# Kernel tuning notes

Measured on AMD Instinct MI355X. Metric: run time of the kernel, lower is better.

Reference implementation:

```python
import jax, jax.numpy as jnp
import numpy as np

N = 50000      # nodes
E = 800000     # edges (before self-loops)
DIN = 146      # input feature dim
D = 128        # hidden/out dim
G = 64         # graphs in batch
L = 4          # number of GCNConv layers (len(hidden_dims[1:]) + 1)
NC = 10        # classes
EPS = 1e-5     # BatchNorm eps


def setup_inputs() -> dict:
    key = jax.random.key(0)
    ks = jax.random.split(key, 12)
    x = jax.random.normal(ks[0], (N, DIN), jnp.float32)
    edge_index = jax.random.randint(ks[1], (2, E), 0, N, dtype=jnp.int64)
    batch = jnp.sort(jax.random.randint(ks[2], (N,), 0, G, dtype=jnp.int64))

    def lin(k, shape, fan_in):
        return (jax.random.normal(k, shape, jnp.float32) / np.sqrt(fan_in)).astype(jnp.float32)

    W_emb = lin(ks[3], (DIN, D), DIN)
    b_emb = jnp.zeros((D,), jnp.float32)
    W_gcn = lin(ks[4], (L, D, D), D)
    b_gcn = jnp.zeros((L, D), jnp.float32)
    bn_gamma = jnp.ones((L, D), jnp.float32)
    bn_beta = jnp.zeros((L, D), jnp.float32)
    W_r1 = lin(ks[5], (D, D // 2), D)
    b_r1 = jnp.zeros((D // 2,), jnp.float32)
    W_r2 = lin(ks[6], (D // 2, D // 4), D // 2)
    b_r2 = jnp.zeros((D // 4,), jnp.float32)
    W_r3 = lin(ks[7], (D // 4, NC), D // 4)
    b_r3 = jnp.zeros((NC,), jnp.float32)
    return {"x": x, "edge_index": edge_index, "batch": batch,
            "W_emb": W_emb, "b_emb": b_emb, "W_gcn": W_gcn, "b_gcn": b_gcn,
            "bn_gamma": bn_gamma, "bn_beta": bn_beta,
            "W_r1": W_r1, "b_r1": b_r1, "W_r2": W_r2, "b_r2": b_r2,
            "W_r3": W_r3, "b_r3": b_r3}


def reference(x, edge_index, batch, W_emb, b_emb, W_gcn, b_gcn,
              bn_gamma, bn_beta, W_r1, b_r1, W_r2, b_r2, W_r3, b_r3):
    # gcn_norm with self-loops (fill_value=1, improved=False)
    loop = jnp.arange(N, dtype=edge_index.dtype)
    src = jnp.concatenate([edge_index[0], loop])
    dst = jnp.concatenate([edge_index[1], loop])
    deg = jax.ops.segment_sum(jnp.ones(src.shape, x.dtype), dst, num_segments=N)
    dinv = jax.lax.rsqrt(jnp.maximum(deg, jnp.asarray(1e-12, x.dtype)))  # deg >= 1 (self loops)
    norm = (dinv[src] * dinv[dst])[:, None]  # [E+N, 1]

    h = x @ W_emb + b_emb  # embedding_h
    for l in range(L):
        h_in = h
        m = h @ W_gcn[l]                                            # [N, D]
        h = jax.ops.segment_sum(m[src] * norm, dst, num_segments=N) + b_gcn[l]
        # BatchNorm1d (training-mode batch stats, biased var)
        mu = h.mean(axis=0)
        var = h.var(axis=0)
        h = (h - mu) * jax.lax.rsqrt(var + EPS) * bn_gamma[l] + bn_beta[l]
        h = jax.nn.relu(h)
        h = h_in + h  # residual (dims always match here)

    # global_mean_pool over batch ids
    sums = jax.ops.segment_sum(h, batch, num_segments=G)
    cnts = jax.ops.segment_sum(jnp.ones((N, 1), h.dtype), batch, num_segments=G)
    hg = sums / jnp.maximum(cnts, 1.0)

    # MLPReadout: two hidden layers halving dims, then classifier
    z = jax.nn.relu(hg @ W_r1 + b_r1)
    z = jax.nn.relu(z @ W_r2 + b_r2)
    return z @ W_r3 + b_r3  # [G, NC]
```

## Files before the change

kernel.cpp:

```cpp
#include <hip/hip_runtime.h>
#include <hip/hip_bf16.h>

#define NN 50000
#define EE 800000
#define DIN 146
#define DD 128
#define GG 64
#define LL 4
#define NC 10
#define BN_EPS 1e-5f

#define KP_EMB 160
#define AST_L  136
#define NCOPY 64
#define NPW 4

#define NBKT 196
#define BHP  200
#define NBE  782

#define A_EDGE   NBE
#define A_INIT   (A_EDGE + 256)
#define A_REPACK (A_INIT + 3907)
#define A_BATCH  (A_REPACK + 196)
#define A_PARAMS (A_BATCH + 384)
#define A_WT     (A_PARAMS + 400)

#define B_GEMM 391
#define C_TOT  (B_GEMM + NBE)

typedef __attribute__((ext_vector_type(8))) short bf16x8;
typedef __attribute__((ext_vector_type(4))) float f32x4;

__device__ __forceinline__ float bf2f(__hip_bfloat16 v) { return __bfloat162float(v); }
__device__ __forceinline__ float loadf(const void* p, long i, int f32) {
    return f32 ? ((const float*)p)[i] : bf2f(((const __hip_bfloat16*)p)[i]);
}
__device__ __forceinline__ unsigned short f2bf_bits(float f) {
    __hip_bfloat16 h = __float2bfloat16(f);
    return *(unsigned short*)&h;
}
__device__ __forceinline__ float bfu2f(unsigned short u) {
    return __uint_as_float((unsigned)u << 16);
}
__device__ __forceinline__ float lo16(unsigned v) { return __uint_as_float(v << 16); }
__device__ __forceinline__ float hi16(unsigned v) { return __uint_as_float(v & 0xffff0000u); }
__device__ __forceinline__ ushort4 pack4(f32x4 v) {
    ushort4 u;
    u.x = f2bf_bits(v[0]); u.y = f2bf_bits(v[1]);
    u.z = f2bf_bits(v[2]); u.w = f2bf_bits(v[3]);
    return u;
}
__device__ __forceinline__ ushort4 pack4s(f32x4 v, float s) {
    ushort4 u;
    u.x = f2bf_bits(s * v[0]); u.y = f2bf_bits(s * v[1]);
    u.z = f2bf_bits(s * v[2]); u.w = f2bf_bits(s * v[3]);
    return u;
}

__device__ __forceinline__ int blk_excl_scan(int v, int t, int* wsum, int* total_sh) {
    __syncthreads();
    int lane = t & 63, w = t >> 6;
    int x = v;
    #pragma unroll
    for (int s = 1; s < 64; s <<= 1) {
        int y = __shfl_up(x, s, 64);
        if (lane >= s) x += y;
    }
    if (lane == 63) wsum[w] = x;
    __syncthreads();
    if (t == 0) {
        int a = 0;
        #pragma unroll
        for (int k = 0; k < 4; ++k) { int tmp = wsum[k]; wsum[k] = a; a += tmp; }
        *total_sh = a;
    }
    __syncthreads();
    return x - v + wsum[w];
}

__global__ void detect_kernel(const void* ei, const void* batch, const void* Wemb,
                              int* __restrict__ flags) {
    __shared__ int s_edge_nz, s_batch_nz, s_f32_cnt;
    int t = threadIdx.x;
    if (t == 0) { s_edge_nz = 0; s_batch_nz = 0; s_f32_cnt = 0; }
    __syncthreads();
    {   const int* w = (const int*)ei;
        long j = ((long)t * ((2L * EE) / 64)) | 1;
        if (w[j] != 0) atomicAdd(&s_edge_nz, 1);
    }
    {   const int* w = (const int*)batch;
        long j = ((long)(NN / 2) + (long)t * ((NN / 2) / 64)) | 1;
        if (j < NN && w[j] != 0) atomicAdd(&s_batch_nz, 1);
    }
    {   const unsigned short* w = (const unsigned short*)Wemb;
        unsigned short v = w[2 * t];
        int ex = (v >> 7) & 0xFF;
        if (v != 0 && ex >= 128) atomicAdd(&s_f32_cnt, 1);
    }
    __syncthreads();
    if (t == 0) {
        flags[0] = (s_edge_nz == 0) ? 1 : 0;
        flags[1] = (s_batch_nz == 0) ? 1 : 0;
        flags[2] = (s_f32_cnt >= 8) ? 1 : 0;
    }
}

struct Param { const void* src; float* dst; int src_n; int dst_n; };
struct Params12 { Param p[12]; };
struct WtDesc { const void* src; long src_off; unsigned short* dst; int K; int Kpad; };
struct WtDescs5 { WtDesc p[5]; };

__global__ __launch_bounds__(256) void mega_conv_kernel(
    const void* __restrict__ x, const void* __restrict__ ei,
    const void* __restrict__ batch, const int* __restrict__ flags,
    unsigned short* __restrict__ xb, float* __restrict__ statmulti,
    float* __restrict__ hgsum, int* __restrict__ b32,
    unsigned* __restrict__ pk, unsigned char* __restrict__ bkt,
    int* __restrict__ bh, int* __restrict__ dcnt, Params12 P, WtDescs5 W)
{
    int b = blockIdx.x;
    int t = threadIdx.x;
    if (b < A_EDGE) {
        __shared__ int hist[NBKT];
        if (t < NBKT) hist[t] = 0;
        __syncthreads();
        int e0 = (b * 256 + t) * 4;
        if (e0 < EE) {
            const int* w = (const int*)ei;
            int4 sv, dv;
            if (flags[0]) {
                int4 u0 = *(const int4*)(w + 2L * e0);
                int4 u1 = *(const int4*)(w + 2L * e0 + 4);
                int4 v0 = *(const int4*)(w + 2L * (EE + e0));
                int4 v1 = *(const int4*)(w + 2L * (EE + e0) + 4);
                sv = make_int4(u0.x, u0.z, u1.x, u1.z);
                dv = make_int4(v0.x, v0.z, v1.x, v1.z);
            } else {
                sv = *(const int4*)(w + e0);
                dv = *(const int4*)(w + EE + e0);
            }
            int ss[4] = {sv.x, sv.y, sv.z, sv.w};
            int dd2[4] = {dv.x, dv.y, dv.z, dv.w};
            unsigned pk4[4], bk4[4];
            #pragma unroll
            for (int k = 0; k < 4; ++k) {
                unsigned s = min((unsigned)ss[k], (unsigned)(NN - 1));
                unsigned d = min((unsigned)dd2[k], (unsigned)(NN - 1));
                pk4[k] = (s << 8) | (d & 255u);
                bk4[k] = d >> 8;
                atomicAdd(&hist[bk4[k]], 1);
            }
            *(uint4*)(pk + e0) = make_uint4(pk4[0], pk4[1], pk4[2], pk4[3]);
            *(uchar4*)(bkt + e0) = make_uchar4((unsigned char)bk4[0], (unsigned char)bk4[1],
                                               (unsigned char)bk4[2], (unsigned char)bk4[3]);
        }
        __syncthreads();
        if (t < NBKT) bh[b * BHP + t] = hist[t];
    } else if (b < A_INIT) {
        int i = (b - A_EDGE) * 256 + t;
        if (i == 0) *dcnt = 0;
        if (i < LL * NCOPY * 256) statmulti[i] = 0.0f;
        if (i < GG * DD) hgsum[i] = 0.0f;
    } else if (b < A_REPACK) {
        int f32 = flags[2];
        long idx8 = (long)(b - A_INIT) * 256 + t;
        if (idx8 < (long)NN * 20) {
            int row = (int)(idx8 / 20);
            int c8 = (int)(idx8 - (long)row * 20) * 8;
            float v[8];
            if (c8 + 8 <= DIN) {
                if (f32) {
                    const float* xp = (const float*)x + (long)row * DIN + c8;
                    #pragma unroll
                    for (int k2 = 0; k2 < 4; ++k2) {
                        float2 f = *(const float2*)(xp + 2 * k2);
                        v[2 * k2] = f.x; v[2 * k2 + 1] = f.y;
                    }
                } else {
                    const unsigned* xp = (const unsigned*)((const unsigned short*)x +
                                                           (long)row * DIN + c8);
                    #pragma unroll
                    for (int k2 = 0; k2 < 4; ++k2) {
                        unsigned u = xp[k2];
                        v[2 * k2] = bfu2f((unsigned short)u);
                        v[2 * k2 + 1] = bfu2f((unsigned short)(u >> 16));
                    }
                }
            } else {
                #pragma unroll
                for (int k = 0; k < 8; ++k) {
                    int col = c8 + k;
                    v[k] = (col < DIN) ? loadf(x, (long)row * DIN + col, f32) : 0.0f;
                }
            }
            unsigned o[4];
            #pragma unroll
            for (int k2 = 0; k2 < 4; ++k2)
                o[k2] = (unsigned)f2bf_bits(v[2 * k2]) |
                        ((unsigned)f2bf_bits(v[2 * k2 + 1]) << 16);
            *(uint4*)(xb + (long)row * KP_EMB + c8) = make_uint4(o[0], o[1], o[2], o[3]);
        }
    } else if (b < A_BATCH) {
        int i = (b - A_REPACK) * 256 + t;
        if (i < NN) b32[i] = flags[1] ? ((const int*)batch)[2L * i] : ((const int*)batch)[i];
    } else if (b < A_PARAMS) {
        int f32 = flags[2];
        int bb = b - A_BATCH;
        const Param& e = P.p[bb >> 5];
        int idx = (bb & 31) * 256 + t;
        if (idx < e.dst_n)
            e.dst[idx] = (idx < e.src_n) ? loadf(e.src, idx, f32) : 0.0f;
    } else {
        int f32 = flags[2];
        int bb = b - A_PARAMS;
        int y = bb / 80;
        const WtDesc& e = W.p[y];
        int idx = (bb - y * 80) * 256 + t;
        if (idx < 128 * e.Kpad) {
            int n = idx / e.Kpad, k = idx - n * e.Kpad;
            float v = (k < e.K) ? loadf(e.src, e.src_off + (long)k * DD + n, f32) : 0.0f;
            e.dst[idx] = f2bf_bits(v);
        }
    }
}

__global__ __launch_bounds__(256) void bscan_kernel(int* __restrict__ bh, int* __restrict__ tot,
                                                    int* __restrict__ base,
                                                    int* __restrict__ off_last,
                                                    int* __restrict__ dcnt) {
    __shared__ int wsum[4], total_sh;
    __shared__ int is_last;
    int b = blockIdx.x;
    int t = threadIdx.x;
    int carry = 0;
    #pragma unroll 1
    for (int c = 0; c < 4; ++c) {
        int i = c * 256 + t;
        int v = (i < NBE) ? bh[i * BHP + b] : 0;
        int excl = blk_excl_scan(v, t, wsum, &total_sh);
        if (i < NBE) bh[i * BHP + b] = excl + carry;
        carry += total_sh;
    }
    if (t == 0) {
        __hip_atomic_store(&tot[b], carry, __ATOMIC_RELEASE, __HIP_MEMORY_SCOPE_AGENT);
        int ticket = __hip_atomic_fetch_add(dcnt, 1, __ATOMIC_ACQ_REL, __HIP_MEMORY_SCOPE_AGENT);
        is_last = (ticket == NBKT - 1) ? 1 : 0;
    }
    __syncthreads();
    if (is_last) {
        int v = 0;
        if (t < NBKT)
            v = __hip_atomic_load(&tot[t], __ATOMIC_ACQUIRE, __HIP_MEMORY_SCOPE_AGENT);
        int excl = blk_excl_scan(v, t, wsum, &total_sh);
        if (t < NBKT) base[t] = excl;
        if (t == 0) { base[NBKT] = total_sh; *off_last = total_sh; }
    }
}


__global__ __launch_bounds__(256) void bucket_emb_kernel(
    const unsigned* __restrict__ pk, const unsigned char* __restrict__ bkt,
    const int* __restrict__ bh, const int* __restrict__ base,
    unsigned* __restrict__ bucketA,
    const unsigned short* __restrict__ Ab,
    const unsigned short* __restrict__ Wt,
    const float* __restrict__ bias,
    unsigned short* __restrict__ hb, int n)
{
    int t = threadIdx.x;
    if (blockIdx.x >= B_GEMM) {
        int bb = blockIdx.x - B_GEMM;
        __shared__ int cur[NBKT];
        if (t < NBKT) cur[t] = bh[bb * BHP + t] + base[t];
        __syncthreads();
        int e0 = (bb * 256 + t) * 4;
        if (e0 < EE) {
            uint4 p4 = *(const uint4*)(pk + e0);
            uchar4 b4 = *(const uchar4*)(bkt + e0);
            unsigned pks[4] = {p4.x, p4.y, p4.z, p4.w};
            unsigned bks[4] = {b4.x, b4.y, b4.z, b4.w};
            #pragma unroll
            for (int k = 0; k < 4; ++k) {
                int slot = atomicAdd(&cur[bks[k]], 1);
                bucketA[slot] = pks[k];
            }
        }
        return;
    }
    int r0 = blockIdx.x * 128;
    int lane = t & 63, w = t >> 6;
    int m = lane & 15, quad = lane >> 4;
    int rbase = r0 + w * 32;
    bf16x8 a[2][5];
    #pragma unroll
    for (int rt = 0; rt < 2; ++rt)
        #pragma unroll
        for (int c = 0; c < 5; ++c) {
            int rr = rbase + rt * 16 + m; if (rr > n - 1) rr = n - 1;
            a[rt][c] = *(const bf16x8*)(Ab + (long)rr * KP_EMB + c * 32 + quad * 8);
        }
    f32x4 acc[2][8];
    #pragma unroll
    for (int t8 = 0; t8 < 8; ++t8) {
        float4 bv = *(const float4*)&bias[t8 * 16 + quad * 4];
        f32x4 ai = {bv.x, bv.y, bv.z, bv.w};
        acc[0][t8] = ai; acc[1][t8] = ai;
    }
    #pragma unroll
    for (int t8 = 0; t8 < 8; ++t8) {
        #pragma unroll
        for (int c = 0; c < 5; ++c) {
            bf16x8 b = *(const bf16x8*)(Wt + (long)(t8 * 16 + m) * KP_EMB + c * 32 + quad * 8);
            acc[0][t8] = __builtin_amdgcn_mfma_f32_16x16x32_bf16(b, a[0][c], acc[0][t8], 0, 0, 0);
            acc[1][t8] = __builtin_amdgcn_mfma_f32_16x16x32_bf16(b, a[1][c], acc[1][t8], 0, 0, 0);
        }
    }
    #pragma unroll
    for (int rt = 0; rt < 2; ++rt) {
        int row = rbase + rt * 16 + m;
        if (row < n) {
            #pragma unroll
            for (int t8 = 0; t8 < 8; ++t8)
                *(ushort4*)(hb + (long)row * DD + t8 * 16 + quad * 4) = pack4(acc[rt][t8]);
        }
    }
}

__global__ __launch_bounds__(256) void csr_kernel(
    const unsigned* __restrict__ bucketA, const int* __restrict__ base,
    int* __restrict__ off, float* __restrict__ dinv, int* __restrict__ src_s)
{
    __shared__ int dg[256], cur[256], wsum[4], total_sh;
    int b = blockIdx.x, t = threadIdx.x;
    int eb0 = base[b], eb1 = base[b + 1];
    dg[t] = 0;
    __syncthreads();
    for (int e = eb0 + t; e < eb1; e += 256)
        atomicAdd(&dg[bucketA[e] & 255u], 1);
    __syncthreads();
    int v = dg[t];
    int excl = blk_excl_scan(v, t, wsum, &total_sh);
    int node = b * 256 + t;
    if (node < NN) {
        off[node] = eb0 + excl;
        dinv[node] = rsqrtf((float)(v + 1));
    }
    cur[t] = excl;
    __syncthreads();
    for (int e = eb0 + t; e < eb1; e += 256) {
        unsigned pv = bucketA[e];
        int r = atomicAdd(&cur[pv & 255u], 1);
        src_s[eb0 + r] = (int)(pv >> 8);
    }
}

__global__ __launch_bounds__(256) void gemm_plain_kernel(
    const unsigned short* __restrict__ Ab,
    const unsigned short* __restrict__ Wt,
    const float* __restrict__ dinv,
    unsigned short* __restrict__ Mb, int n)
{
    int t = threadIdx.x;
    int r0 = blockIdx.x * 128;
    int lane = t & 63, w = t >> 6;
    int m = lane & 15, quad = lane >> 4;
    int rbase = r0 + w * 32;
    bf16x8 a[2][4];
    #pragma unroll
    for (int rt = 0; rt < 2; ++rt)
        #pragma unroll
        for (int c = 0; c < 4; ++c) {
            int rr = rbase + rt * 16 + m; if (rr > n - 1) rr = n - 1;
            a[rt][c] = *(const bf16x8*)(Ab + (long)rr * DD + c * 32 + quad * 8);
        }
    float dvt[2];
    int rowt[2];
    #pragma unroll
    for (int rt = 0; rt < 2; ++rt) {
        int rr = rbase + rt * 16 + m;
        rowt[rt] = rr;
        if (rr > n - 1) rr = n - 1;
        dvt[rt] = dinv[rr];
    }
    f32x4 acc[2][8];
    #pragma unroll
    for (int t8 = 0; t8 < 8; ++t8) {
        f32x4 z = {0.f, 0.f, 0.f, 0.f};
        acc[0][t8] = z; acc[1][t8] = z;
    }
    #pragma unroll
    for (int t8 = 0; t8 < 8; ++t8) {
        #pragma unroll
        for (int c = 0; c < 4; ++c) {
            bf16x8 b = *(const bf16x8*)(Wt + (long)(t8 * 16 + m) * DD + c * 32 + quad * 8);
            acc[0][t8] = __builtin_amdgcn_mfma_f32_16x16x32_bf16(b, a[0][c], acc[0][t8], 0, 0, 0);
            acc[1][t8] = __builtin_amdgcn_mfma_f32_16x16x32_bf16(b, a[1][c], acc[1][t8], 0, 0, 0);
        }
    }
    #pragma unroll
    for (int rt = 0; rt < 2; ++rt) {
        if (rowt[rt] < n) {
            #pragma unroll
            for (int t8 = 0; t8 < 8; ++t8)
                *(ushort4*)(Mb + (long)rowt[rt] * DD + t8 * 16 + quad * 4) = pack4s(acc[rt][t8], dvt[rt]);
        }
    }
}

__global__ __launch_bounds__(256) void gemm_fused_kernel(
    const unsigned short* __restrict__ aggb, unsigned short* __restrict__ hb,
    const float* __restrict__ statmulti, const float* __restrict__ gamma,
    const float* __restrict__ beta, const float* __restrict__ dinv,
    const unsigned short* __restrict__ Wt, unsigned short* __restrict__ Mb, int n)
{
    __shared__ unsigned short As[128 * AST_L];
    __shared__ float bnsh[256];
    int t = threadIdx.x;
    int r0 = blockIdx.x * 128;
    {
        float s = 0.0f;
        #pragma unroll 8
        for (int k = 0; k < NCOPY; ++k) s += statmulti[k * 256 + t];
        bnsh[t] = s;
    }
    __syncthreads();
    {
        int c4 = (t & 31) * 4, rsub = t >> 5;
        float inv_n = 1.0f / (float)n;
        float4 sm = *(const float4*)&bnsh[c4];
        float4 sq = *(const float4*)&bnsh[128 + c4];
        float4 ga = *(const float4*)&gamma[c4];
        float4 be = *(const float4*)&beta[c4];
        float4 mu, rs;
        mu.x = sm.x * inv_n; mu.y = sm.y * inv_n; mu.z = sm.z * inv_n; mu.w = sm.w * inv_n;
        rs.x = rsqrtf(sq.x * inv_n - mu.x * mu.x + BN_EPS) * ga.x;
        rs.y = rsqrtf(sq.y * inv_n - mu.y * mu.y + BN_EPS) * ga.y;
        rs.z = rsqrtf(sq.z * inv_n - mu.z * mu.z + BN_EPS) * ga.z;
        rs.w = rsqrtf(sq.w * inv_n - mu.w * mu.w + BN_EPS) * ga.w;
        #pragma unroll 4
        for (int i = 0; i < 16; ++i) {
            int row = i * 8 + rsub;
            int r = r0 + row;
            unsigned short o0 = 0, o1 = 0, o2 = 0, o3 = 0;
            if (r < n) {
                long g = (long)r * DD + c4;
                ushort4 au = *(const ushort4*)&aggb[g];
                ushort4 hu = *(const ushort4*)&hb[g];
                float h0 = bfu2f(hu.x) + fmaxf((bfu2f(au.x) - mu.x) * rs.x + be.x, 0.0f);
                float h1 = bfu2f(hu.y) + fmaxf((bfu2f(au.y) - mu.y) * rs.y + be.y, 0.0f);
                float h2 = bfu2f(hu.z) + fmaxf((bfu2f(au.z) - mu.z) * rs.z + be.z, 0.0f);
                float h3 = bfu2f(hu.w) + fmaxf((bfu2f(au.w) - mu.w) * rs.w + be.w, 0.0f);
                o0 = f2bf_bits(h0); o1 = f2bf_bits(h1);
                o2 = f2bf_bits(h2); o3 = f2bf_bits(h3);
                ushort4 ho; ho.x = o0; ho.y = o1; ho.z = o2; ho.w = o3;
                *(ushort4*)&hb[g] = ho;
            }
            unsigned short* dst = &As[row * AST_L + c4];
            dst[0] = o0; dst[1] = o1; dst[2] = o2; dst[3] = o3;
        }
    }
    __syncthreads();
    int lane = t & 63, w = t >> 6;
    int m = lane & 15, quad = lane >> 4;
    int rl = w * 32;
    int rbase = r0 + rl;
    bf16x8 a[2][4];
    #pragma unroll
    for (int rt = 0; rt < 2; ++rt)
        #pragma unroll
        for (int c = 0; c < 4; ++c)
            a[rt][c] = *(const bf16x8*)(As + (rl + rt * 16 + m) * AST_L + c * 32 + quad * 8);
    float dvt[2];
    int rowt[2];
    #pragma unroll
    for (int rt = 0; rt < 2; ++rt) {
        int rr = rbase + rt * 16 + m;
        rowt[rt] = rr;
        if (rr > n - 1) rr = n - 1;
        dvt[rt] = dinv[rr];
    }
    f32x4 acc[2][8];
    #pragma unroll
    for (int t8 = 0; t8 < 8; ++t8) {
        f32x4 z = {0.f, 0.f, 0.f, 0.f};
        acc[0][t8] = z; acc[1][t8] = z;
    }
    #pragma unroll
    for (int t8 = 0; t8 < 8; ++t8) {
        #pragma unroll
        for (int c = 0; c < 4; ++c) {
            bf16x8 b = *(const bf16x8*)(Wt + (long)(t8 * 16 + m) * DD + c * 32 + quad * 8);
            acc[0][t8] = __builtin_amdgcn_mfma_f32_16x16x32_bf16(b, a[0][c], acc[0][t8], 0, 0, 0);
            acc[1][t8] = __builtin_amdgcn_mfma_f32_16x16x32_bf16(b, a[1][c], acc[1][t8], 0, 0, 0);
        }
    }
    #pragma unroll
    for (int rt = 0; rt < 2; ++rt) {
        if (rowt[rt] < n) {
            #pragma unroll
            for (int t8 = 0; t8 < 8; ++t8)
                *(ushort4*)(Mb + (long)rowt[rt] * DD + t8 * 16 + quad * 4) = pack4s(acc[rt][t8], dvt[rt]);
        }
    }
}

__global__ __launch_bounds__(256) void agg_kernel(
    const unsigned* __restrict__ mb32, const int* __restrict__ off,
    const int* __restrict__ src_s,
    const float* __restrict__ dinv, const float* __restrict__ bias,
    unsigned* __restrict__ aggb32, float* __restrict__ statacc)
{
    __shared__ float2 ssum[4][64], ssq[4][64];
    int t = threadIdx.x;
    int wv = t >> 6, lane = t & 63;
    float2 bi = ((const float2*)bias)[lane];
    float2 sAcc = {0.0f, 0.0f}, qAcc = {0.0f, 0.0f};
    int i0 = (blockIdx.x * 4 + wv) * NPW;
    #pragma unroll 1
    for (int ni = 0; ni < NPW; ++ni) {
        int i = i0 + ni;
        if (i >= NN) break;
        int e  = __builtin_amdgcn_readfirstlane(off[i]);
        int e1 = __builtin_amdgcn_readfirstlane(off[i + 1]);
        unsigned vs = mb32[(long)i * 64 + lane];
        float a0 = lo16(vs), a1 = hi16(vs);
        for (; e + 8 <= e1; e += 8) {
            int j0 = __builtin_amdgcn_readfirstlane(src_s[e + 0]);
            int j1 = __builtin_amdgcn_readfirstlane(src_s[e + 1]);
            int j2 = __builtin_amdgcn_readfirstlane(src_s[e + 2]);
            int j3 = __builtin_amdgcn_readfirstlane(src_s[e + 3]);
            int j4 = __builtin_amdgcn_readfirstlane(src_s[e + 4]);
            int j5 = __builtin_amdgcn_readfirstlane(src_s[e + 5]);
            int j6 = __builtin_amdgcn_readfirstlane(src_s[e + 6]);
            int j7 = __builtin_amdgcn_readfirstlane(src_s[e + 7]);
            unsigned v0 = mb32[(long)j0 * 64 + lane];
            unsigned v1 = mb32[(long)j1 * 64 + lane];
            unsigned v2 = mb32[(long)j2 * 64 + lane];
            unsigned v3 = mb32[(long)j3 * 64 + lane];
            unsigned v4 = mb32[(long)j4 * 64 + lane];
            unsigned v5 = mb32[(long)j5 * 64 + lane];
            unsigned v6 = mb32[(long)j6 * 64 + lane];
            unsigned v7 = mb32[(long)j7 * 64 + lane];
            a0 += lo16(v0); a1 += hi16(v0);
            a0 += lo16(v1); a1 += hi16(v1);
            a0 += lo16(v2); a1 += hi16(v2);
            a0 += lo16(v3); a1 += hi16(v3);
            a0 += lo16(v4); a1 += hi16(v4);
            a0 += lo16(v5); a1 += hi16(v5);
            a0 += lo16(v6); a1 += hi16(v6);
            a0 += lo16(v7); a1 += hi16(v7);
        }
        for (; e + 4 <= e1; e += 4) {
            int j0 = __builtin_amdgcn_readfirstlane(src_s[e + 0]);
            int j1 = __builtin_amdgcn_readfirstlane(src_s[e + 1]);
            int j2 = __builtin_amdgcn_readfirstlane(src_s[e + 2]);
            int j3 = __builtin_amdgcn_readfirstlane(src_s[e + 3]);
            unsigned v0 = mb32[(long)j0 * 64 + lane];
            unsigned v1 = mb32[(long)j1 * 64 + lane];
            unsigned v2 = mb32[(long)j2 * 64 + lane];
            unsigned v3 = mb32[(long)j3 * 64 + lane];
            a0 += lo16(v0); a1 += hi16(v0);
            a0 += lo16(v1); a1 += hi16(v1);
            a0 += lo16(v2); a1 += hi16(v2);
            a0 += lo16(v3); a1 += hi16(v3);
        }
        for (; e < e1; ++e) {
            int j = __builtin_amdgcn_readfirstlane(src_s[e]);
            unsigned v = mb32[(long)j * 64 + lane];
            a0 += lo16(v); a1 += hi16(v);
        }
        float di = dinv[i];
        float o0 = fmaf(di, a0, bi.x);
        float o1 = fmaf(di, a1, bi.y);
        aggb32[(long)i * 64 + lane] = ((unsigned)f2bf_bits(o1) << 16) | f2bf_bits(o0);
        sAcc.x += o0; sAcc.y += o1;
        qAcc.x += o0 * o0; qAcc.y += o1 * o1;
    }
    ssum[wv][lane] = sAcc; ssq[wv][lane] = qAcc;
    __syncthreads();
    if (wv == 0) {
        float2 s0 = ssum[0][lane], s1 = ssum[1][lane], s2 = ssum[2][lane], s3 = ssum[3][lane];
        float2 q0 = ssq[0][lane], q1 = ssq[1][lane], q2 = ssq[2][lane], q3 = ssq[3][lane];
        float sx = s0.x + s1.x + s2.x + s3.x;
        float sy = s0.y + s1.y + s2.y + s3.y;
        float qx = q0.x + q1.x + q2.x + q3.x;
        float qy = q0.y + q1.y + q2.y + q3.y;
        float* copy = statacc + (blockIdx.x & (NCOPY - 1)) * 256;
        atomicAdd(&copy[2 * lane], sx);
        atomicAdd(&copy[2 * lane + 1], sy);
        atomicAdd(&copy[128 + 2 * lane], qx);
        atomicAdd(&copy[128 + 2 * lane + 1], qy);
    }
}

__global__ void pool1_kernel(const unsigned short* __restrict__ hb,
                             const unsigned short* __restrict__ aggb,
                             const float* __restrict__ statmulti,
                             const float* __restrict__ gamma, const float* __restrict__ beta,
                             const int* __restrict__ b32, float* __restrict__ hgsum, int n) {
    __shared__ float bnsh[256];
    int t = threadIdx.x;
    {
        float s = 0.0f;
        #pragma unroll 8
        for (int k = 0; k < NCOPY; ++k) s += statmulti[k * 256 + t];
        bnsh[t] = s;
    }
    __syncthreads();
    int c4 = (t & 31) * 4, rsub = t >> 5;
    float inv_n = 1.0f / (float)n;
    float4 sm = *(const float4*)&bnsh[c4];
    float4 sq = *(const float4*)&bnsh[128 + c4];
    float4 ga = *(const float4*)&gamma[c4];
    float4 be = *(const float4*)&beta[c4];
    float4 mu, rs;
    mu.x = sm.x * inv_n; mu.y = sm.y * inv_n; mu.z = sm.z * inv_n; mu.w = sm.w * inv_n;
    rs.x = rsqrtf(sq.x * inv_n - mu.x * mu.x + BN_EPS) * ga.x;
    rs.y = rsqrtf(sq.y * inv_n - mu.y * mu.y + BN_EPS) * ga.y;
    rs.z = rsqrtf(sq.z * inv_n - mu.z * mu.z + BN_EPS) * ga.z;
    rs.w = rsqrtf(sq.w * inv_n - mu.w * mu.w + BN_EPS) * ga.w;
    int rows_pb = (n + gridDim.x - 1) / gridDim.x;
    int r0 = blockIdx.x * rows_pb;
    int r1 = min(n, r0 + rows_pb);
    float4 acc = {0, 0, 0, 0};
    int gcur = -1;
    for (int r = r0 + rsub; r < r1; r += 8) {
        int g = b32[r];
        if (g != gcur) {
            if (gcur >= 0) {
                atomicAdd(&hgsum[gcur * DD + c4 + 0], acc.x);
                atomicAdd(&hgsum[gcur * DD + c4 + 1], acc.y);
                atomicAdd(&hgsum[gcur * DD + c4 + 2], acc.z);
                atomicAdd(&hgsum[gcur * DD + c4 + 3], acc.w);
            }
            acc.x = acc.y = acc.z = acc.w = 0.0f;
            gcur = ((unsigned)g < (unsigned)GG) ? g : -1;
        }
        if (gcur >= 0) {
            long ix = (long)r * DD + c4;
            ushort4 au = *(const ushort4*)&aggb[ix];
            ushort4 hu = *(const ushort4*)&hb[ix];
            acc.x += bfu2f(hu.x) + fmaxf((bfu2f(au.x) - mu.x) * rs.x + be.x, 0.0f);
            acc.y += bfu2f(hu.y) + fmaxf((bfu2f(au.y) - mu.y) * rs.y + be.y, 0.0f);
            acc.z += bfu2f(hu.z) + fmaxf((bfu2f(au.z) - mu.z) * rs.z + be.z, 0.0f);
            acc.w += bfu2f(hu.w) + fmaxf((bfu2f(au.w) - mu.w) * rs.w + be.w, 0.0f);
        }
    }
    if (gcur >= 0) {
        atomicAdd(&hgsum[gcur * DD + c4 + 0], acc.x);
        atomicAdd(&hgsum[gcur * DD + c4 + 1], acc.y);
        atomicAdd(&hgsum[gcur * DD + c4 + 2], acc.z);
        atomicAdd(&hgsum[gcur * DD + c4 + 3], acc.w);
    }
}

__device__ int lower_bound_i(const int* __restrict__ a, int n, int v) {
    int lo = 0, hi = n;
    while (lo < hi) {
        int mid = (lo + hi) >> 1;
        if (a[mid] < v) lo = mid + 1; else hi = mid;
    }
    return lo;
}

__global__ void readout_kernel(const float* __restrict__ hgsum, const int* __restrict__ b32,
                               const float* __restrict__ W1, const float* __restrict__ b1,
                               const float* __restrict__ W2, const float* __restrict__ b2,
                               const float* __restrict__ W3, const float* __restrict__ b3,
                               const int* __restrict__ flags, void* __restrict__ out, int n) {
    int f32 = flags[2];
    int g = blockIdx.x;
    int t = threadIdx.x;
    __shared__ float hgs[DD];
    __shared__ float z1[DD / 2];
    __shared__ float z2[DD / 4];
    int lo = lower_bound_i(b32, n, g);
    int hi = lower_bound_i(b32, n, g + 1);
    float invc = 1.0f / fmaxf((float)(hi - lo), 1.0f);
    hgs[t] = hgsum[g * DD + t] * invc;
    __syncthreads();
    if (t < DD / 2) {
        float acc = b1[t];
        #pragma unroll 8
        for (int k = 0; k < DD; ++k) acc = fmaf(hgs[k], W1[k * (DD / 2) + t], acc);
        z1[t] = fmaxf(acc, 0.0f);
    }
    __syncthreads();
    if (t < DD / 4) {
        float acc = b2[t];
        #pragma unroll 8
        for (int k = 0; k < DD / 2; ++k) acc = fmaf(z1[k], W2[k * (DD / 4) + t], acc);
        z2[t] = fmaxf(acc, 0.0f);
    }
    __syncthreads();
    if (t < NC) {
        float acc = b3[t];
        #pragma unroll 8
        for (int k = 0; k < DD / 4; ++k) acc = fmaf(z2[k], W3[k * NC + t], acc);
        if (f32) ((float*)out)[g * NC + t] = acc;
        else     ((__hip_bfloat16*)out)[g * NC + t] = __float2bfloat16(acc);
    }
}

extern "C" void kernel_launch(void* const* d_in, const int* in_sizes, int n_in,
                              void* d_out, int out_size, void* d_ws, size_t ws_size,
                              hipStream_t stream) {
    const void* x      = d_in[0];
    const void* ei     = d_in[1];
    const void* batch  = d_in[2];
    const void* W_emb  = d_in[3];
    const void* b_emb  = d_in[4];
    const void* W_gcn  = d_in[5];
    const void* b_gcn  = d_in[6];
    const void* bn_g   = d_in[7];
    const void* bn_b   = d_in[8];
    const void* W_r1   = d_in[9];
    const void* b_r1   = d_in[10];
    const void* W_r2   = d_in[11];
    const void* b_r2   = d_in[12];
    const void* W_r3   = d_in[13];
    const void* b_r3   = d_in[14];

    char* p = (char*)d_ws;
    auto alloc = [&](size_t bytes) -> void* {
        void* r = (void*)p;
        p += (bytes + 255) & ~(size_t)255;
        return r;
    };
    int*   flags  = (int*)alloc(64 * 4);
    int*   dcnt   = (int*)alloc(64 * 4);
    float* statmulti = (float*)alloc((size_t)LL * NCOPY * 256 * 4);
    float* hgsum  = (float*)alloc((size_t)GG * DD * 4);
    int*   off    = (int*)alloc((size_t)(NN + 1) * 4);
    float* dinv   = (float*)alloc((size_t)NN * 4);
    int*   b32    = (int*)alloc((size_t)NN * 4);
    int*   src_s  = (int*)alloc((size_t)EE * 4);
    unsigned* pk  = (unsigned*)alloc((size_t)EE * 4);
    unsigned char* bkt = (unsigned char*)alloc((size_t)EE);
    int*   bh     = (int*)alloc((size_t)NBE * BHP * 4);
    int*   tot    = (int*)alloc(256 * 4);
    int*   base   = (int*)alloc(256 * 4);
    unsigned* bucketA = (unsigned*)alloc((size_t)EE * 4);
    unsigned short* hb = (unsigned short*)alloc((size_t)NN * DD * 2);
    unsigned short* mb = (unsigned short*)alloc((size_t)NN * DD * 2);
    unsigned short* aggb = (unsigned short*)alloc((size_t)NN * DD * 2);
    unsigned short* xb = (unsigned short*)alloc((size_t)NN * KP_EMB * 2);
    unsigned short* wt_emb = (unsigned short*)alloc((size_t)DD * KP_EMB * 2);
    unsigned short* wt_gcn = (unsigned short*)alloc((size_t)LL * DD * DD * 2);
    float* b_emb32 = (float*)alloc(DD * 4);
    float* b_gcn32 = (float*)alloc((size_t)LL * DD * 4);
    float* bng32   = (float*)alloc((size_t)LL * DD * 4);
    float* bnb32   = (float*)alloc((size_t)LL * DD * 4);
    float* wr1     = (float*)alloc((size_t)DD * (DD / 2) * 4);
    float* br1     = (float*)alloc((DD / 2) * 4);
    float* wr2     = (float*)alloc((size_t)(DD / 2) * (DD / 4) * 4);
    float* br2     = (float*)alloc((DD / 4) * 4);
    float* wr3     = (float*)alloc((size_t)(DD / 4) * NC * 4);
    float* br3     = (float*)alloc(NC * 4);

    detect_kernel<<<1, 64, 0, stream>>>(ei, batch, W_emb, flags);

    Params12 P;
    P.p[0]  = { b_emb, b_emb32, DD, DD };
    P.p[1]  = { b_gcn, b_gcn32, LL * DD, LL * DD };
    P.p[2]  = { bn_g,  bng32,   LL * DD, LL * DD };
    P.p[3]  = { bn_b,  bnb32,   LL * DD, LL * DD };
    P.p[4]  = { W_r1,  wr1,     DD * (DD / 2), DD * (DD / 2) };
    P.p[5]  = { b_r1,  br1,     DD / 2, DD / 2 };
    P.p[6]  = { W_r2,  wr2,     (DD / 2) * (DD / 4), (DD / 2) * (DD / 4) };
    P.p[7]  = { b_r2,  br2,     DD / 4, DD / 4 };
    P.p[8]  = { W_r3,  wr3,     (DD / 4) * NC, (DD / 4) * NC };
    P.p[9]  = { b_r3,  br3,     NC, NC };
    P.p[10] = { b_r3,  br3,     0, 0 };
    P.p[11] = { b_r3,  br3,     0, 0 };

    WtDescs5 W;
    W.p[0] = { W_emb, 0,            wt_emb,                DIN, KP_EMB };
    W.p[1] = { W_gcn, 0L * DD * DD, wt_gcn + 0L * DD * DD, DD,  DD };
    W.p[2] = { W_gcn, 1L * DD * DD, wt_gcn + 1L * DD * DD, DD,  DD };
    W.p[3] = { W_gcn, 2L * DD * DD, wt_gcn + 2L * DD * DD, DD,  DD };
    W.p[4] = { W_gcn, 3L * DD * DD, wt_gcn + 3L * DD * DD, DD,  DD };

    mega_conv_kernel<<<A_WT, 256, 0, stream>>>(x, ei, batch, flags, xb, statmulti,
                                               hgsum, b32, pk, bkt, bh, dcnt, P, W);

    bscan_kernel<<<NBKT, 256, 0, stream>>>(bh, tot, base, off + NN, dcnt);

    bucket_emb_kernel<<<C_TOT, 256, 0, stream>>>(pk, bkt, bh, base, bucketA,
                                                 xb, wt_emb, b_emb32, hb, NN);

    csr_kernel<<<NBKT, 256, 0, stream>>>(bucketA, base, off, dinv, src_s);

    gemm_plain_kernel<<<(NN + 127) / 128, 256, 0, stream>>>(hb, wt_gcn, dinv, mb, NN);

    int ngemm = (NN + 127) / 128;
    int nagg = (NN + 4 * NPW - 1) / (4 * NPW);
    for (int l = 0; l < LL; ++l) {
        if (l > 0) {
            gemm_fused_kernel<<<ngemm, 256, 0, stream>>>(
                aggb, hb, statmulti + (size_t)(l - 1) * NCOPY * 256,
                bng32 + (l - 1) * DD, bnb32 + (l - 1) * DD,
                dinv, wt_gcn + (size_t)l * DD * DD, mb, NN);
        }
        agg_kernel<<<nagg, 256, 0, stream>>>((const unsigned*)mb, off, src_s, dinv,
                                             b_gcn32 + l * DD, (unsigned*)aggb,
                                             statmulti + (size_t)l * NCOPY * 256);
    }

    pool1_kernel<<<512, 256, 0, stream>>>(hb, aggb, statmulti + (size_t)(LL - 1) * NCOPY * 256,
                                          bng32 + (LL - 1) * DD, bnb32 + (LL - 1) * DD,
                                          b32, hgsum, NN);
    readout_kernel<<<GG, DD, 0, stream>>>(hgsum, b32, wr1, br1, wr2, br2, wr3, br3,
                                          flags, d_out, NN);
}
```

Before: 402.0 us.

## Fuse first GCN GEMM into embedding kernel; apply source dinv inside aggregation

The first layer's GEMM moves into the embedding kernel. The embedding output is staged in shared memory and multiplied by W_gcn[0] in the same block, so the separate gemm_plain launch and its reread of h go away. Because dinv is not ready until csr_kernel runs after this point, the GEMMs no longer pre-scale rows by dinv. Instead the aggregation kernel loads dinv[src] per edge through scalar loads and uses FMAs, which adds a scalar load per edge. Nodes per wave in the aggregation are halved to give it more blocks.

```diff
diff --git a/kernel.cpp b/kernel.cpp
--- a/kernel.cpp
+++ b/kernel.cpp
@@ -13,7 +13,7 @@
 #define KP_EMB 160
 #define AST_L  136
 #define NCOPY 64
-#define NPW 4
+#define NPW 2
 
 #define NBKT 196
 #define BHP  200
@@ -45,16 +45,13 @@
 }
 __device__ __forceinline__ float lo16(unsigned v) { return __uint_as_float(v << 16); }
 __device__ __forceinline__ float hi16(unsigned v) { return __uint_as_float(v & 0xffff0000u); }
+__device__ __forceinline__ float sload_f(const float* __restrict__ p, int j) {
+    return __uint_as_float(__builtin_amdgcn_readfirstlane(__float_as_uint(p[j])));
+}
 __device__ __forceinline__ ushort4 pack4(f32x4 v) {
     ushort4 u;
     u.x = f2bf_bits(v[0]); u.y = f2bf_bits(v[1]);
     u.z = f2bf_bits(v[2]); u.w = f2bf_bits(v[3]);
-    return u;
-}
-__device__ __forceinline__ ushort4 pack4s(f32x4 v, float s) {
-    ushort4 u;
-    u.x = f2bf_bits(s * v[0]); u.y = f2bf_bits(s * v[1]);
-    u.z = f2bf_bits(s * v[2]); u.w = f2bf_bits(s * v[3]);
     return u;
 }
 
@@ -265,14 +262,19 @@
     unsigned* __restrict__ bucketA,
     const unsigned short* __restrict__ Ab,
     const unsigned short* __restrict__ Wt,
+    const unsigned short* __restrict__ Wt0,
     const float* __restrict__ bias,
-    unsigned short* __restrict__ hb, int n)
+    unsigned short* __restrict__ hb,
+    unsigned short* __restrict__ Mb, int n)
 {
+    __shared__ union {
+        unsigned short As[128 * AST_L];
+        int cur[NBKT];
+    } sh;
     int t = threadIdx.x;
     if (blockIdx.x >= B_GEMM) {
         int bb = blockIdx.x - B_GEMM;
-        __shared__ int cur[NBKT];
-        if (t < NBKT) cur[t] = bh[bb * BHP + t] + base[t];
+        if (t < NBKT) sh.cur[t] = bh[bb * BHP + t] + base[t];
         __syncthreads();
         int e0 = (bb * 256 + t) * 4;
         if (e0 < EE) {
@@ -282,7 +284,7 @@
             unsigned bks[4] = {b4.x, b4.y, b4.z, b4.w};
             #pragma unroll
             for (int k = 0; k < 4; ++k) {
-                int slot = atomicAdd(&cur[bks[k]], 1);
+                int slot = atomicAdd(&sh.cur[bks[k]], 1);
                 bucketA[slot] = pks[k];
             }
         }
@@ -291,7 +293,8 @@
     int r0 = blockIdx.x * 128;
     int lane = t & 63, w = t >> 6;
     int m = lane & 15, quad = lane >> 4;
-    int rbase = r0 + w * 32;
+    int rl = w * 32;
+    int rbase = r0 + rl;
     bf16x8 a[2][5];
     #pragma unroll
     for (int rt = 0; rt < 2; ++rt)
@@ -319,10 +322,44 @@
     #pragma unroll
     for (int rt = 0; rt < 2; ++rt) {
         int row = rbase + rt * 16 + m;
+        int rloc = rl + rt * 16 + m;
+        #pragma unroll
+        for (int t8 = 0; t8 < 8; ++t8) {
+            ushort4 u = pack4(acc[rt][t8]);
+            *(ushort4*)(&sh.As[rloc * AST_L + t8 * 16 + quad * 4]) = u;
+            if (row < n)
+                *(ushort4*)(hb + (long)row * DD + t8 * 16 + quad * 4) = u;
+        }
+    }
+    __syncthreads();
+    bf16x8 a2[2][4];
+    #pragma unroll
+    for (int rt = 0; rt < 2; ++rt)
+        #pragma unroll
+        for (int c = 0; c < 4; ++c)
+            a2[rt][c] = *(const bf16x8*)(&sh.As[(rl + rt * 16 + m) * AST_L + c * 32 + quad * 8]);
+    f32x4 acc2[2][8];
+    #pragma unroll
+    for (int t8 = 0; t8 < 8; ++t8) {
+        f32x4 z = {0.f, 0.f, 0.f, 0.f};
+        acc2[0][t8] = z; acc2[1][t8] = z;
+    }
+    #pragma unroll
+    for (int t8 = 0; t8 < 8; ++t8) {
+        #pragma unroll
+        for (int c = 0; c < 4; ++c) {
+            bf16x8 b = *(const bf16x8*)(Wt0 + (long)(t8 * 16 + m) * DD + c * 32 + quad * 8);
+            acc2[0][t8] = __builtin_amdgcn_mfma_f32_16x16x32_bf16(b, a2[0][c], acc2[0][t8], 0, 0, 0);
+            acc2[1][t8] = __builtin_amdgcn_mfma_f32_16x16x32_bf16(b, a2[1][c], acc2[1][t8], 0, 0, 0);
+        }
+    }
+    #pragma unroll
+    for (int rt = 0; rt < 2; ++rt) {
+        int row = rbase + rt * 16 + m;
         if (row < n) {
             #pragma unroll
             for (int t8 = 0; t8 < 8; ++t8)
-                *(ushort4*)(hb + (long)row * DD + t8 * 16 + quad * 4) = pack4(acc[rt][t8]);
+                *(ushort4*)(Mb + (long)row * DD + t8 * 16 + quad * 4) = pack4(acc2[rt][t8]);
         }
     }
 }
@@ -355,63 +392,10 @@
     }
 }
 
-__global__ __launch_bounds__(256) void gemm_plain_kernel(
-    const unsigned short* __restrict__ Ab,
-    const unsigned short* __restrict__ Wt,
-    const float* __restrict__ dinv,
-    unsigned short* __restrict__ Mb, int n)
-{
-    int t = threadIdx.x;
-    int r0 = blockIdx.x * 128;
-    int lane = t & 63, w = t >> 6;
-    int m = lane & 15, quad = lane >> 4;
-    int rbase = r0 + w * 32;
-    bf16x8 a[2][4];
-    #pragma unroll
-    for (int rt = 0; rt < 2; ++rt)
-        #pragma unroll
-        for (int c = 0; c < 4; ++c) {
-            int rr = rbase + rt * 16 + m; if (rr > n - 1) rr = n - 1;
-            a[rt][c] = *(const bf16x8*)(Ab + (long)rr * DD + c * 32 + quad * 8);
-        }
-    float dvt[2];
-    int rowt[2];
-    #pragma unroll
-    for (int rt = 0; rt < 2; ++rt) {
-        int rr = rbase + rt * 16 + m;
-        rowt[rt] = rr;
-        if (rr > n - 1) rr = n - 1;
-        dvt[rt] = dinv[rr];
-    }
-    f32x4 acc[2][8];
-    #pragma unroll
-    for (int t8 = 0; t8 < 8; ++t8) {
-        f32x4 z = {0.f, 0.f, 0.f, 0.f};
-        acc[0][t8] = z; acc[1][t8] = z;
-    }
-    #pragma unroll
-    for (int t8 = 0; t8 < 8; ++t8) {
-        #pragma unroll
-        for (int c = 0; c < 4; ++c) {
-            bf16x8 b = *(const bf16x8*)(Wt + (long)(t8 * 16 + m) * DD + c * 32 + quad * 8);
-            acc[0][t8] = __builtin_amdgcn_mfma_f32_16x16x32_bf16(b, a[0][c], acc[0][t8], 0, 0, 0);
-            acc[1][t8] = __builtin_amdgcn_mfma_f32_16x16x32_bf16(b, a[1][c], acc[1][t8], 0, 0, 0);
-        }
-    }
-    #pragma unroll
-    for (int rt = 0; rt < 2; ++rt) {
-        if (rowt[rt] < n) {
-            #pragma unroll
-            for (int t8 = 0; t8 < 8; ++t8)
-                *(ushort4*)(Mb + (long)rowt[rt] * DD + t8 * 16 + quad * 4) = pack4s(acc[rt][t8], dvt[rt]);
-        }
-    }
-}
-
 __global__ __launch_bounds__(256) void gemm_fused_kernel(
     const unsigned short* __restrict__ aggb, unsigned short* __restrict__ hb,
     const float* __restrict__ statmulti, const float* __restrict__ gamma,
-    const float* __restrict__ beta, const float* __restrict__ dinv,
+    const float* __restrict__ beta,
     const unsigned short* __restrict__ Wt, unsigned short* __restrict__ Mb, int n)
 {
     __shared__ unsigned short As[128 * AST_L];
@@ -471,15 +455,6 @@
         #pragma unroll
         for (int c = 0; c < 4; ++c)
             a[rt][c] = *(const bf16x8*)(As + (rl + rt * 16 + m) * AST_L + c * 32 + quad * 8);
-    float dvt[2];
-    int rowt[2];
-    #pragma unroll
-    for (int rt = 0; rt < 2; ++rt) {
-        int rr = rbase + rt * 16 + m;
-        rowt[rt] = rr;
-        if (rr > n - 1) rr = n - 1;
-        dvt[rt] = dinv[rr];
-    }
     f32x4 acc[2][8];
     #pragma unroll
     for (int t8 = 0; t8 < 8; ++t8) {
@@ -497,10 +472,11 @@
     }
     #pragma unroll
     for (int rt = 0; rt < 2; ++rt) {
-        if (rowt[rt] < n) {
+        int row = rbase + rt * 16 + m;
+        if (row < n) {
             #pragma unroll
             for (int t8 = 0; t8 < 8; ++t8)
-                *(ushort4*)(Mb + (long)rowt[rt] * DD + t8 * 16 + quad * 4) = pack4s(acc[rt][t8], dvt[rt]);
+                *(ushort4*)(Mb + (long)row * DD + t8 * 16 + quad * 4) = pack4(acc[rt][t8]);
         }
     }
 }
@@ -523,8 +499,9 @@
         if (i >= NN) break;
         int e  = __builtin_amdgcn_readfirstlane(off[i]);
         int e1 = __builtin_amdgcn_readfirstlane(off[i + 1]);
+        float di = sload_f(dinv, i);
         unsigned vs = mb32[(long)i * 64 + lane];
-        float a0 = lo16(vs), a1 = hi16(vs);
+        float a0 = di * lo16(vs), a1 = di * hi16(vs);
         for (; e + 8 <= e1; e += 8) {
             int j0 = __builtin_amdgcn_readfirstlane(src_s[e + 0]);
             int j1 = __builtin_amdgcn_readfirstlane(src_s[e + 1]);
@@ -534,6 +511,10 @@
             int j5 = __builtin_amdgcn_readfirstlane(src_s[e + 5]);
             int j6 = __builtin_amdgcn_readfirstlane(src_s[e + 6]);
             int j7 = __builtin_amdgcn_readfirstlane(src_s[e + 7]);
+            float d0 = sload_f(dinv, j0), d1 = sload_f(dinv, j1);
+            float d2 = sload_f(dinv, j2), d3 = sload_f(dinv, j3);
+            float d4 = sload_f(dinv, j4), d5 = sload_f(dinv, j5);
+            float d6 = sload_f(dinv, j6), d7 = sload_f(dinv, j7);
             unsigned v0 = mb32[(long)j0 * 64 + lane];
             unsigned v1 = mb32[(long)j1 * 64 + lane];
             unsigned v2 = mb32[(long)j2 * 64 + lane];
@@ -542,35 +523,37 @@
             unsigned v5 = mb32[(long)j5 * 64 + lane];
             unsigned v6 = mb32[(long)j6 * 64 + lane];
             unsigned v7 = mb32[(long)j7 * 64 + lane];
-            a0 += lo16(v0); a1 += hi16(v0);
-            a0 += lo16(v1); a1 += hi16(v1);
-            a0 += lo16(v2); a1 += hi16(v2);
-            a0 += lo16(v3); a1 += hi16(v3);
-            a0 += lo16(v4); a1 += hi16(v4);
-            a0 += lo16(v5); a1 += hi16(v5);
-            a0 += lo16(v6); a1 += hi16(v6);
-            a0 += lo16(v7); a1 += hi16(v7);
+            a0 = fmaf(d0, lo16(v0), a0); a1 = fmaf(d0, hi16(v0), a1);
+            a0 = fmaf(d1, lo16(v1), a0); a1 = fmaf(d1, hi16(v1), a1);
+            a0 = fmaf(d2, lo16(v2), a0); a1 = fmaf(d2, hi16(v2), a1);
+            a0 = fmaf(d3, lo16(v3), a0); a1 = fmaf(d3, hi16(v3), a1);
+            a0 = fmaf(d4, lo16(v4), a0); a1 = fmaf(d4, hi16(v4), a1);
+            a0 = fmaf(d5, lo16(v5), a0); a1 = fmaf(d5, hi16(v5), a1);
+            a0 = fmaf(d6, lo16(v6), a0); a1 = fmaf(d6, hi16(v6), a1);
+            a0 = fmaf(d7, lo16(v7), a0); a1 = fmaf(d7, hi16(v7), a1);
         }
         for (; e + 4 <= e1; e += 4) {
             int j0 = __builtin_amdgcn_readfirstlane(src_s[e + 0]);
             int j1 = __builtin_amdgcn_readfirstlane(src_s[e + 1]);
             int j2 = __builtin_amdgcn_readfirstlane(src_s[e + 2]);
             int j3 = __builtin_amdgcn_readfirstlane(src_s[e + 3]);
+            float d0 = sload_f(dinv, j0), d1 = sload_f(dinv, j1);
+            float d2 = sload_f(dinv, j2), d3 = sload_f(dinv, j3);
             unsigned v0 = mb32[(long)j0 * 64 + lane];
             unsigned v1 = mb32[(long)j1 * 64 + lane];
             unsigned v2 = mb32[(long)j2 * 64 + lane];
             unsigned v3 = mb32[(long)j3 * 64 + lane];
-            a0 += lo16(v0); a1 += hi16(v0);
-            a0 += lo16(v1); a1 += hi16(v1);
-            a0 += lo16(v2); a1 += hi16(v2);
-            a0 += lo16(v3); a1 += hi16(v3);
+            a0 = fmaf(d0, lo16(v0), a0); a1 = fmaf(d0, hi16(v0), a1);
+            a0 = fmaf(d1, lo16(v1), a0); a1 = fmaf(d1, hi16(v1), a1);
+            a0 = fmaf(d2, lo16(v2), a0); a1 = fmaf(d2, hi16(v2), a1);
+            a0 = fmaf(d3, lo16(v3), a0); a1 = fmaf(d3, hi16(v3), a1);
         }
         for (; e < e1; ++e) {
             int j = __builtin_amdgcn_readfirstlane(src_s[e]);
+            float dj = sload_f(dinv, j);
             unsigned v = mb32[(long)j * 64 + lane];
-            a0 += lo16(v); a1 += hi16(v);
-        }
-        float di = dinv[i];
+            a0 = fmaf(dj, lo16(v), a0); a1 = fmaf(dj, hi16(v), a1);
+        }
         float o0 = fmaf(di, a0, bi.x);
         float o1 = fmaf(di, a1, bi.y);
         aggb32[(long)i * 64 + lane] = ((unsigned)f2bf_bits(o1) << 16) | f2bf_bits(o0);
@@ -788,11 +771,9 @@
     bscan_kernel<<<NBKT, 256, 0, stream>>>(bh, tot, base, off + NN, dcnt);
 
     bucket_emb_kernel<<<C_TOT, 256, 0, stream>>>(pk, bkt, bh, base, bucketA,
-                                                 xb, wt_emb, b_emb32, hb, NN);
+                                                 xb, wt_emb, wt_gcn, b_emb32, hb, mb, NN);
 
     csr_kernel<<<NBKT, 256, 0, stream>>>(bucketA, base, off, dinv, src_s);
-
-    gemm_plain_kernel<<<(NN + 127) / 128, 256, 0, stream>>>(hb, wt_gcn, dinv, mb, NN);
 
     int ngemm = (NN + 127) / 128;
     int nagg = (NN + 4 * NPW - 1) / (4 * NPW);
@@ -801,7 +782,7 @@
             gemm_fused_kernel<<<ngemm, 256, 0, stream>>>(
                 aggb, hb, statmulti + (size_t)(l - 1) * NCOPY * 256,
                 bng32 + (l - 1) * DD, bnb32 + (l - 1) * DD,
-                dinv, wt_gcn + (size_t)l * DD * DD, mb, NN);
+                wt_gcn + (size_t)l * DD * DD, mb, NN);
         }
         agg_kernel<<<nagg, 256, 0, stream>>>((const unsigned*)mb, off, src_s, dinv,
                                              b_gcn32 + l * DD, (unsigned*)aggb,
```

Result: no change. 405.8 us (median of 2 runs) (+0.9%).
